# Optimization experiments

Measured on AMD Instinct MI355X. Metric: run time of the kernel, lower is better.

Reference implementation:

```python
import jax, jax.numpy as jnp
import numpy as np

D_MODEL = 256
NHEAD = 8
DHEAD = D_MODEL // NHEAD
LN_EPS = 1e-5
ATTN_EPS = 1e-6


def layer_norm(x, gamma, beta):
    mu = jnp.mean(x, axis=-1, keepdims=True)
    var = jnp.mean(jnp.square(x - mu), axis=-1, keepdims=True)
    return (x - mu) * jax.lax.rsqrt(var + LN_EPS) * gamma + beta


def setup_inputs() -> dict:
    key = jax.random.key(0)
    ks = jax.random.split(key, 12)
    B, L, S = 8, 4096, 4096
    s = 1.0 / np.sqrt(D_MODEL)
    return {
        "x": jax.random.normal(ks[0], (B, L, D_MODEL), jnp.float32),
        "source": jax.random.normal(ks[1], (B, S, D_MODEL), jnp.float32),
        "wq": jax.random.normal(ks[2], (D_MODEL, D_MODEL), jnp.float32) * s,
        "wk": jax.random.normal(ks[3], (D_MODEL, D_MODEL), jnp.float32) * s,
        "wv": jax.random.normal(ks[4], (D_MODEL, D_MODEL), jnp.float32) * s,
        "wmerge": jax.random.normal(ks[5], (D_MODEL, D_MODEL), jnp.float32) * s,
        "w1": jax.random.normal(ks[6], (2 * D_MODEL, D_MODEL), jnp.float32) * s,
        "w2": jax.random.normal(ks[7], (D_MODEL, 2 * D_MODEL), jnp.float32) * (1.0 / np.sqrt(2 * D_MODEL)),
        "g1": jnp.ones((D_MODEL,), jnp.float32),
        "b1": jnp.zeros((D_MODEL,), jnp.float32),
        "g2": jnp.ones((D_MODEL,), jnp.float32),
        "b2": jnp.zeros((D_MODEL,), jnp.float32),
    }


def reference(x, source, wq, wk, wv, wmerge, w1, w2, g1, b1, g2, b2):
    B, L, _ = x.shape
    S = source.shape[1]
    # QKV projections (bias-free Linear: y = x @ W^T), split into heads
    q = (x @ wq.T).reshape(B, L, NHEAD, DHEAD)
    k = (source @ wk.T).reshape(B, S, NHEAD, DHEAD)
    v = (source @ wv.T).reshape(B, S, NHEAD, DHEAD)
    # LinearAttention (LoFTR): feature map elu(.)+1, kernelized attention
    Q = jax.nn.elu(q) + 1.0
    K = jax.nn.elu(k) + 1.0
    v_len = jnp.asarray(S, v.dtype)
    values = v / v_len
    KV = jnp.einsum('bshd,bshv->bhdv', K, values)        # [B,H,D,D]
    Z = 1.0 / (jnp.einsum('blhd,bhd->blh', Q, K.sum(axis=1)) + ATTN_EPS)
    attended = jnp.einsum('blhd,bhdv,blh->blhv', Q, KV, Z) * v_len
    # merge + residual LN
    message = attended.reshape(B, L, D_MODEL) @ wmerge.T
    x = x + layer_norm(message, g1, b1)
    # MLP (d -> 2d -> d, ReLU) + residual LN
    h = jax.nn.relu(x @ w1.T) @ w2.T
    x = x + layer_norm(h, g2, b2)
    return x
```

## Files before the change

### kernel.cpp

```cpp
#include <hip/hip_runtime.h>
#include <hip/hip_bf16.h>

#define DM 256
#define SEQ 4096
#define XSTR 528
#define KSTR 144

typedef __attribute__((ext_vector_type(8))) short bf16x8;
typedef __attribute__((ext_vector_type(4))) float f32x4;

#define MFMA16(a, b, c) __builtin_amdgcn_mfma_f32_16x16x32_bf16(a, b, c, 0, 0, 0)

__device__ __forceinline__ short f2bf(float f) {
    union { __hip_bfloat16 h; short s; } u;
    u.h = __float2bfloat16(f);
    return u.s;
}
__device__ __forceinline__ float bf2f(short s) {
    union { unsigned u; float f; } c; c.u = ((unsigned)(unsigned short)s) << 16; return c.f;
}
__device__ __forceinline__ bf16x8 pack8(float4 a, float4 b) {
    bf16x8 r;
    r[0] = f2bf(a.x); r[1] = f2bf(a.y); r[2] = f2bf(a.z); r[3] = f2bf(a.w);
    r[4] = f2bf(b.x); r[5] = f2bf(b.y); r[6] = f2bf(b.z); r[7] = f2bf(b.w);
    return r;
}

__global__ __launch_bounds__(256) void kWconv(const float* __restrict__ wq, const float* __restrict__ wk,
                                              const float* __restrict__ wv, const float* __restrict__ wm,
                                              const float* __restrict__ w1, const float* __restrict__ w2,
                                              short* __restrict__ dstws, float* __restrict__ kva,
                                              float* __restrict__ ksum) {
    int blk = blockIdx.x;
    int gid = blk * 256 + threadIdx.x;
    kva[gid] = 0.f;
    if (gid < 2048) ksum[gid] = 0.f;
    const float* src; short* dst;
    if (blk < 32)       { src = wq; dst = dstws;          }
    else if (blk < 64)  { src = wk; dst = dstws + 65536;  blk -= 32; }
    else if (blk < 96)  { src = wv; dst = dstws + 131072; blk -= 64; }
    else if (blk < 128) { src = wm; dst = dstws + 196608; blk -= 96; }
    else if (blk < 192) { src = w1; dst = dstws + 262144; blk -= 128; }
    else                { src = w2; dst = dstws + 393216; blk -= 192; }
    int idx = (blk * 256 + threadIdx.x) * 8;
    float4 f0 = *(const float4*)(src + idx), f1 = *(const float4*)(src + idx + 4);
    *(bf16x8*)(dst + idx) = pack8(f0, f1);
}

__global__ __launch_bounds__(512, 4) void kA(const float* __restrict__ src,
                                             const short* __restrict__ wk, const short* __restrict__ wv,
                                             float* __restrict__ kva, float* __restrict__ ksum) {
    __shared__ char lds[73728];
    int t = threadIdx.x, lane = t & 63, w = t >> 6, r16 = lane & 15, g = lane >> 4;
    int b = blockIdx.x >> 6, blk = blockIdx.x & 63;
    const float* S = src + ((size_t)b * SEQ + blk * 64) * DM;
#pragma unroll
    for (int i = 0; i < 4; i++) {
        int chunk = t + i * 512, row = chunk >> 5, c8 = chunk & 31;
        const float* p = S + row * DM + c8 * 8;
        float4 f0 = *(const float4*)p, f1 = *(const float4*)(p + 4);
        *(bf16x8*)(lds + row * XSTR + c8 * 16) = pack8(f0, f1);
    }
    __syncthreads();
    f32x4 zz = {0.f, 0.f, 0.f, 0.f};
    f32x4 ak[4][2], av[4][2];
#pragma unroll
    for (int mi = 0; mi < 4; mi++)
#pragma unroll
        for (int ni = 0; ni < 2; ni++) { ak[mi][ni] = zz; av[mi][ni] = zz; }
    const char* aB0 = lds + r16 * XSTR + g * 16;
    const short* wkB0 = wk + (w * 32 + r16) * DM + g * 8;
    const short* wvB0 = wv + (w * 32 + r16) * DM + g * 8;
#pragma unroll
    for (int kt = 0; kt < 8; kt++) {
        bf16x8 A[4];
#pragma unroll
        for (int mi = 0; mi < 4; mi++)
            A[mi] = *(const bf16x8*)(aB0 + mi * (16 * XSTR) + kt * 64);
#pragma unroll
        for (int ni = 0; ni < 2; ni++) {
            bf16x8 Bk = *(const bf16x8*)(wkB0 + ni * (16 * DM) + kt * 32);
            bf16x8 Bv = *(const bf16x8*)(wvB0 + ni * (16 * DM) + kt * 32);
#pragma unroll
            for (int mi = 0; mi < 4; mi++) {
                ak[mi][ni] = MFMA16(A[mi], Bk, ak[mi][ni]);
                av[mi][ni] = MFMA16(A[mi], Bv, av[mi][ni]);
            }
        }
    }
    __syncthreads();
    char* kT = lds + w * 9216;
    char* vT = kT + 4608;
    float ksp[2] = {0.f, 0.f};
#pragma unroll
    for (int mi = 0; mi < 4; mi++)
#pragma unroll
        for (int ni = 0; ni < 2; ni++)
#pragma unroll
            for (int j = 0; j < 4; j++) {
                float q = ak[mi][ni][j];
                float e = q > 0.f ? q + 1.f : __expf(q);
                ksp[ni] += e;
                int srow = mi * 16 + g * 4 + j, feat = ni * 16 + r16;
                int by = feat * KSTR + srow * 2;
                *(short*)(kT + by) = f2bf(e);
                *(short*)(vT + by) = f2bf(av[mi][ni][j]);
            }
    __syncthreads();
    f32x4 kv[2][2];
#pragma unroll
    for (int vi = 0; vi < 2; vi++)
#pragma unroll
        for (int di = 0; di < 2; di++) kv[vi][di] = zz;
    {
        const char* vB = vT + r16 * KSTR + g * 16;
        const char* kB = kT + r16 * KSTR + g * 16;
#pragma unroll
        for (int st = 0; st < 2; st++) {
            bf16x8 Af[2], Bf[2];
#pragma unroll
            for (int vi = 0; vi < 2; vi++) {
                Af[vi] = *(const bf16x8*)(vB + vi * (16 * KSTR) + st * 64);
                Bf[vi] = *(const bf16x8*)(kB + vi * (16 * KSTR) + st * 64);
            }
#pragma unroll
            for (int vi = 0; vi < 2; vi++)
#pragma unroll
                for (int di = 0; di < 2; di++) kv[vi][di] = MFMA16(Af[vi], Bf[di], kv[vi][di]);
        }
    }
    float* kvp = kva + (size_t)(b * 8 + w) * 1024;
#pragma unroll
    for (int vi = 0; vi < 2; vi++)
#pragma unroll
        for (int di = 0; di < 2; di++)
#pragma unroll
            for (int j = 0; j < 4; j++) {
                int v = vi * 16 + g * 4 + j, d = di * 16 + r16;
                atomicAdd(&kvp[v * 32 + d], kv[vi][di][j]);
            }
#pragma unroll
    for (int ni = 0; ni < 2; ni++) {
        ksp[ni] += __shfl_xor(ksp[ni], 16);
        ksp[ni] += __shfl_xor(ksp[ni], 32);
    }
    if (lane < 16) {
#pragma unroll
        for (int ni = 0; ni < 2; ni++)
            atomicAdd(&ksum[(b * 8 + w) * 32 + ni * 16 + lane], ksp[ni]);
    }
}

__global__ __launch_bounds__(512, 4) void kBC(const float* __restrict__ x,
                                              const short* __restrict__ wq_bf, const short* __restrict__ wm_bf,
                                              const short* __restrict__ w1_bf, const short* __restrict__ w2_bf,
                                              const float* __restrict__ kva, const float* __restrict__ ksum,
                                              const float* __restrict__ g1, const float* __restrict__ b1,
                                              const float* __restrict__ g2, const float* __restrict__ b2,
                                              float* __restrict__ out) {
    __shared__ char lds[72704];
    char* xt = lds;
    char* qa = lds + 33792;
    float* red = (float*)(lds + 67584);
    float* ksl = (float*)(lds + 71680);
    int t = threadIdx.x, lane = t & 63, w = t >> 6, r16 = lane & 15, g = lane >> 4;
    int b = blockIdx.x >> 6, lb = blockIdx.x & 63, l0 = lb * 64;
    const float* xb = x + ((size_t)b * SEQ + l0) * DM;
#pragma unroll
    for (int i = 0; i < 4; i++) {
        int chunk = t + i * 512, row = chunk >> 5, c8 = chunk & 31;
        const float* p = xb + row * DM + c8 * 8;
        float4 f0 = *(const float4*)p, f1 = *(const float4*)(p + 4);
        *(bf16x8*)(xt + row * XSTR + c8 * 16) = pack8(f0, f1);
    }
    if (t < 256) ksl[t] = ksum[b * 256 + t];
    __syncthreads();
    f32x4 zz = {0.f, 0.f, 0.f, 0.f};
    const char* aXB = xt + r16 * XSTR + g * 16;
    const char* aQB = qa + r16 * XSTR + g * 16;
    f32x4 acc[4][2];
#pragma unroll
    for (int mi = 0; mi < 4; mi++)
#pragma unroll
        for (int ni = 0; ni < 2; ni++) acc[mi][ni] = zz;
    {
        const short* wqB = wq_bf + (w * 32 + r16) * DM + g * 8;
#pragma unroll
        for (int kt = 0; kt < 8; kt++) {
            bf16x8 A[4], Bf[2];
#pragma unroll
            for (int mi = 0; mi < 4; mi++)
                A[mi] = *(const bf16x8*)(aXB + mi * (16 * XSTR) + kt * 64);
#pragma unroll
            for (int ni = 0; ni < 2; ni++)
                Bf[ni] = *(const bf16x8*)(wqB + ni * (16 * DM) + kt * 32);
#pragma unroll
            for (int mi = 0; mi < 4; mi++)
#pragma unroll
                for (int ni = 0; ni < 2; ni++) acc[mi][ni] = MFMA16(A[mi], Bf[ni], acc[mi][ni]);
        }
    }
    float ks0 = ksl[w * 32 + r16], ks1 = ksl[w * 32 + 16 + r16];
    float Zr[4][4];
#pragma unroll
    for (int mi = 0; mi < 4; mi++)
#pragma unroll
        for (int j = 0; j < 4; j++) {
#pragma unroll
            for (int ni = 0; ni < 2; ni++) {
                float q = acc[mi][ni][j];
                acc[mi][ni][j] = q > 0.f ? q + 1.f : __expf(q);
            }
            float d0 = acc[mi][0][j] * ks0 + acc[mi][1][j] * ks1;
#pragma unroll
            for (int m = 1; m < 16; m <<= 1) d0 += __shfl_xor(d0, m);
            Zr[mi][j] = 1.f / (d0 + 1e-6f);
        }
#pragma unroll
    for (int mi = 0; mi < 4; mi++)
#pragma unroll
        for (int ni = 0; ni < 2; ni++)
#pragma unroll
            for (int j = 0; j < 4; j++) {
                int row = mi * 16 + g * 4 + j, col = w * 32 + ni * 16 + r16;
                *(short*)(qa + row * XSTR + col * 2) = f2bf(acc[mi][ni][j]);
            }
    f32x4 at[4][2];
#pragma unroll
    for (int mi = 0; mi < 4; mi++)
#pragma unroll
        for (int vi = 0; vi < 2; vi++) at[mi][vi] = zz;
    {
        bf16x8 A2[4], B2[2];
#pragma unroll
        for (int mi = 0; mi < 4; mi++)
            A2[mi] = *(const bf16x8*)(qa + (mi * 16 + r16) * XSTR + (w * 32 + g * 8) * 2);
        const float* kvb = kva + (size_t)(b * 8 + w) * 1024;
#pragma unroll
        for (int vi = 0; vi < 2; vi++) {
            const float* p = kvb + (vi * 16 + r16) * 32 + g * 8;
            float4 f0 = *(const float4*)p, f1 = *(const float4*)(p + 4);
            B2[vi] = pack8(f0, f1);
        }
#pragma unroll
        for (int mi = 0; mi < 4; mi++)
#pragma unroll
            for (int vi = 0; vi < 2; vi++) at[mi][vi] = MFMA16(A2[mi], B2[vi], at[mi][vi]);
    }
#pragma unroll
    for (int mi = 0; mi < 4; mi++)
#pragma unroll
        for (int vi = 0; vi < 2; vi++)
#pragma unroll
            for (int j = 0; j < 4; j++) {
                int row = mi * 16 + g * 4 + j, col = w * 32 + vi * 16 + r16;
                *(short*)(qa + row * XSTR + col * 2) = f2bf(at[mi][vi][j] * Zr[mi][j]);
            }
    __syncthreads();
    f32x4 am[4][2];
#pragma unroll
    for (int mi = 0; mi < 4; mi++)
#pragma unroll
        for (int ni = 0; ni < 2; ni++) am[mi][ni] = zz;
    {
        const short* wmB = wm_bf + (w * 32 + r16) * DM + g * 8;
#pragma unroll
        for (int kt = 0; kt < 8; kt++) {
            bf16x8 A[4], Bf[2];
#pragma unroll
            for (int mi = 0; mi < 4; mi++)
                A[mi] = *(const bf16x8*)(aQB + mi * (16 * XSTR) + kt * 64);
#pragma unroll
            for (int ni = 0; ni < 2; ni++)
                Bf[ni] = *(const bf16x8*)(wmB + ni * (16 * DM) + kt * 32);
#pragma unroll
            for (int mi = 0; mi < 4; mi++)
#pragma unroll
                for (int ni = 0; ni < 2; ni++) am[mi][ni] = MFMA16(A[mi], Bf[ni], am[mi][ni]);
        }
    }
#pragma unroll
    for (int mi = 0; mi < 4; mi++)
#pragma unroll
        for (int j = 0; j < 4; j++) {
            float s = am[mi][0][j] + am[mi][1][j];
            float s2 = am[mi][0][j] * am[mi][0][j] + am[mi][1][j] * am[mi][1][j];
#pragma unroll
            for (int m = 1; m < 16; m <<= 1) { s += __shfl_xor(s, m); s2 += __shfl_xor(s2, m); }
            if (r16 == 0) { int row = mi * 16 + g * 4 + j; red[(row * 8 + w) * 2] = s; red[(row * 8 + w) * 2 + 1] = s2; }
        }
    __syncthreads();
    {
        float g1v[2], b1v[2];
#pragma unroll
        for (int ni = 0; ni < 2; ni++) { int col = w * 32 + ni * 16 + r16; g1v[ni] = g1[col]; b1v[ni] = b1[col]; }
#pragma unroll
        for (int mi = 0; mi < 4; mi++)
#pragma unroll
            for (int j = 0; j < 4; j++) {
                int row = mi * 16 + g * 4 + j;
                float mu = 0.f, ex2 = 0.f;
#pragma unroll
                for (int ww = 0; ww < 8; ww++) { mu += red[(row * 8 + ww) * 2]; ex2 += red[(row * 8 + ww) * 2 + 1]; }
                mu *= (1.f / DM); ex2 *= (1.f / DM);
                float rstd = rsqrtf(ex2 - mu * mu + 1e-5f);
#pragma unroll
                for (int ni = 0; ni < 2; ni++) {
                    int col = w * 32 + ni * 16 + r16;
                    char* bp = xt + row * XSTR + col * 2;
                    float xv = bf2f(*(const short*)bp);
                    *(short*)bp = f2bf(xv + (am[mi][ni][j] - mu) * rstd * g1v[ni] + b1v[ni]);
                }
            }
    }
    __syncthreads();
    f32x4 a2[4][2];
#pragma unroll
    for (int mi = 0; mi < 4; mi++)
#pragma unroll
        for (int ni = 0; ni < 2; ni++) a2[mi][ni] = zz;
#pragma unroll
    for (int hf = 0; hf < 2; hf++) {
        f32x4 a1[4][2];
#pragma unroll
        for (int mi = 0; mi < 4; mi++)
#pragma unroll
            for (int ni = 0; ni < 2; ni++) a1[mi][ni] = zz;
        {
            const short* w1B = w1_bf + (hf * 256 + w * 32 + r16) * DM + g * 8;
#pragma unroll
            for (int kt = 0; kt < 8; kt++) {
                bf16x8 A[4], Bf[2];
#pragma unroll
                for (int mi = 0; mi < 4; mi++)
                    A[mi] = *(const bf16x8*)(aXB + mi * (16 * XSTR) + kt * 64);
#pragma unroll
                for (int ni = 0; ni < 2; ni++)
                    Bf[ni] = *(const bf16x8*)(w1B + ni * (16 * DM) + kt * 32);
#pragma unroll
                for (int mi = 0; mi < 4; mi++)
#pragma unroll
                    for (int ni = 0; ni < 2; ni++) a1[mi][ni] = MFMA16(A[mi], Bf[ni], a1[mi][ni]);
            }
        }
#pragma unroll
        for (int mi = 0; mi < 4; mi++)
#pragma unroll
            for (int ni = 0; ni < 2; ni++)
#pragma unroll
                for (int j = 0; j < 4; j++) {
                    float hv = a1[mi][ni][j]; hv = hv > 0.f ? hv : 0.f;
                    int row = mi * 16 + g * 4 + j, col = w * 32 + ni * 16 + r16;
                    *(short*)(qa + row * XSTR + col * 2) = f2bf(hv);
                }
        __syncthreads();
        {
            const short* w2B = w2_bf + (w * 32 + r16) * 512 + hf * 256 + g * 8;
#pragma unroll
            for (int kt = 0; kt < 8; kt++) {
                bf16x8 A[4], Bf[2];
#pragma unroll
                for (int mi = 0; mi < 4; mi++)
                    A[mi] = *(const bf16x8*)(aQB + mi * (16 * XSTR) + kt * 64);
#pragma unroll
                for (int ni = 0; ni < 2; ni++)
                    Bf[ni] = *(const bf16x8*)(w2B + ni * (16 * 512) + kt * 32);
#pragma unroll
                for (int mi = 0; mi < 4; mi++)
#pragma unroll
                    for (int ni = 0; ni < 2; ni++) a2[mi][ni] = MFMA16(A[mi], Bf[ni], a2[mi][ni]);
            }
        }
        __syncthreads();
    }
#pragma unroll
    for (int mi = 0; mi < 4; mi++)
#pragma unroll
        for (int j = 0; j < 4; j++) {
            float s = a2[mi][0][j] + a2[mi][1][j];
            float s2 = a2[mi][0][j] * a2[mi][0][j] + a2[mi][1][j] * a2[mi][1][j];
#pragma unroll
            for (int m = 1; m < 16; m <<= 1) { s += __shfl_xor(s, m); s2 += __shfl_xor(s2, m); }
            if (r16 == 0) { int row = mi * 16 + g * 4 + j; red[(row * 8 + w) * 2] = s; red[(row * 8 + w) * 2 + 1] = s2; }
        }
    __syncthreads();
    {
        float g2v[2], b2v[2];
#pragma unroll
        for (int ni = 0; ni < 2; ni++) { int col = w * 32 + ni * 16 + r16; g2v[ni] = g2[col]; b2v[ni] = b2[col]; }
        float* op = out + ((size_t)b * SEQ + l0) * DM;
#pragma unroll
        for (int mi = 0; mi < 4; mi++)
#pragma unroll
            for (int j = 0; j < 4; j++) {
                int row = mi * 16 + g * 4 + j;
                float mu = 0.f, ex2 = 0.f;
#pragma unroll
                for (int ww = 0; ww < 8; ww++) { mu += red[(row * 8 + ww) * 2]; ex2 += red[(row * 8 + ww) * 2 + 1]; }
                mu *= (1.f / DM); ex2 *= (1.f / DM);
                float rstd = rsqrtf(ex2 - mu * mu + 1e-5f);
#pragma unroll
                for (int ni = 0; ni < 2; ni++) {
                    int col = w * 32 + ni * 16 + r16;
                    float xv = bf2f(*(const short*)(xt + row * XSTR + col * 2));
                    op[row * DM + col] = xv + (a2[mi][ni][j] - mu) * rstd * g2v[ni] + b2v[ni];
                }
            }
    }
}

extern "C" void kernel_launch(void* const* d_in, const int* in_sizes, int n_in,
                              void* d_out, int out_size, void* d_ws, size_t ws_size,
                              hipStream_t stream) {
    const float* x   = (const float*)d_in[0];
    const float* src = (const float*)d_in[1];
    const float* wq  = (const float*)d_in[2];
    const float* wk  = (const float*)d_in[3];
    const float* wv  = (const float*)d_in[4];
    const float* wm  = (const float*)d_in[5];
    const float* w1  = (const float*)d_in[6];
    const float* w2  = (const float*)d_in[7];
    const float* g1  = (const float*)d_in[8];
    const float* b1  = (const float*)d_in[9];
    const float* g2  = (const float*)d_in[10];
    const float* b2  = (const float*)d_in[11];
    float* out = (float*)d_out;

    char* ws = (char*)d_ws;
    short* w_bf = (short*)ws;
    float* kva  = (float*)(ws + 1048576);
    float* ksum = (float*)(ws + 1310720);

    kWconv<<<256, 256, 0, stream>>>(wq, wk, wv, wm, w1, w2, w_bf, kva, ksum);
    kA<<<512, 512, 0, stream>>>(src, w_bf + 65536, w_bf + 131072, kva, ksum);
    kBC<<<512, 512, 0, stream>>>(x, w_bf, w_bf + 196608, w_bf + 262144, w_bf + 393216,
                                 kva, ksum, g1, b1, g2, b2, out);
}
```

Measured before the change: 218.0 us.

## Halve kA row tile, prefetch weight fragments in kBC GEMMs, inline bf16 rounding

```diff
diff --git a/kernel.cpp b/kernel.cpp
--- a/kernel.cpp
+++ b/kernel.cpp
@@ -4,7 +4,7 @@
 #define DM 256
 #define SEQ 4096
 #define XSTR 528
-#define KSTR 144
+#define TSTR 72
 
 typedef __attribute__((ext_vector_type(8))) short bf16x8;
 typedef __attribute__((ext_vector_type(4))) float f32x4;
@@ -12,9 +12,9 @@
 #define MFMA16(a, b, c) __builtin_amdgcn_mfma_f32_16x16x32_bf16(a, b, c, 0, 0, 0)
 
 __device__ __forceinline__ short f2bf(float f) {
-    union { __hip_bfloat16 h; short s; } u;
-    u.h = __float2bfloat16(f);
-    return u.s;
+    union { float f; unsigned u; } c; c.f = f;
+    unsigned r = (c.u + 0x7FFFu + ((c.u >> 16) & 1u)) >> 16;
+    return (short)r;
 }
 __device__ __forceinline__ float bf2f(short s) {
     union { unsigned u; float f; } c; c.u = ((unsigned)(unsigned short)s) << 16; return c.f;
@@ -50,12 +50,12 @@
 __global__ __launch_bounds__(512, 4) void kA(const float* __restrict__ src,
                                              const short* __restrict__ wk, const short* __restrict__ wv,
                                              float* __restrict__ kva, float* __restrict__ ksum) {
-    __shared__ char lds[73728];
+    __shared__ char lds[36864];
     int t = threadIdx.x, lane = t & 63, w = t >> 6, r16 = lane & 15, g = lane >> 4;
-    int b = blockIdx.x >> 6, blk = blockIdx.x & 63;
-    const float* S = src + ((size_t)b * SEQ + blk * 64) * DM;
-#pragma unroll
-    for (int i = 0; i < 4; i++) {
+    int b = blockIdx.x >> 7, blk = blockIdx.x & 127;
+    const float* S = src + ((size_t)b * SEQ + blk * 32) * DM;
+#pragma unroll
+    for (int i = 0; i < 2; i++) {
         int chunk = t + i * 512, row = chunk >> 5, c8 = chunk & 31;
         const float* p = S + row * DM + c8 * 8;
         float4 f0 = *(const float4*)p, f1 = *(const float4*)(p + 4);
@@ -63,9 +63,9 @@
     }
     __syncthreads();
     f32x4 zz = {0.f, 0.f, 0.f, 0.f};
-    f32x4 ak[4][2], av[4][2];
-#pragma unroll
-    for (int mi = 0; mi < 4; mi++)
+    f32x4 ak[2][2], av[2][2];
+#pragma unroll
+    for (int mi = 0; mi < 2; mi++)
 #pragma unroll
         for (int ni = 0; ni < 2; ni++) { ak[mi][ni] = zz; av[mi][ni] = zz; }
     const char* aB0 = lds + r16 * XSTR + g * 16;
@@ -73,27 +73,27 @@
     const short* wvB0 = wv + (w * 32 + r16) * DM + g * 8;
 #pragma unroll
     for (int kt = 0; kt < 8; kt++) {
-        bf16x8 A[4];
-#pragma unroll
-        for (int mi = 0; mi < 4; mi++)
+        bf16x8 A[2];
+#pragma unroll
+        for (int mi = 0; mi < 2; mi++)
             A[mi] = *(const bf16x8*)(aB0 + mi * (16 * XSTR) + kt * 64);
 #pragma unroll
         for (int ni = 0; ni < 2; ni++) {
             bf16x8 Bk = *(const bf16x8*)(wkB0 + ni * (16 * DM) + kt * 32);
             bf16x8 Bv = *(const bf16x8*)(wvB0 + ni * (16 * DM) + kt * 32);
 #pragma unroll
-            for (int mi = 0; mi < 4; mi++) {
+            for (int mi = 0; mi < 2; mi++) {
                 ak[mi][ni] = MFMA16(A[mi], Bk, ak[mi][ni]);
                 av[mi][ni] = MFMA16(A[mi], Bv, av[mi][ni]);
             }
         }
     }
     __syncthreads();
-    char* kT = lds + w * 9216;
-    char* vT = kT + 4608;
+    char* kT = lds + w * 4608;
+    char* vT = kT + 2304;
     float ksp[2] = {0.f, 0.f};
 #pragma unroll
-    for (int mi = 0; mi < 4; mi++)
+    for (int mi = 0; mi < 2; mi++)
 #pragma unroll
         for (int ni = 0; ni < 2; ni++)
 #pragma unroll
@@ -102,7 +102,7 @@
                 float e = q > 0.f ? q + 1.f : __expf(q);
                 ksp[ni] += e;
                 int srow = mi * 16 + g * 4 + j, feat = ni * 16 + r16;
-                int by = feat * KSTR + srow * 2;
+                int by = feat * TSTR + srow * 2;
                 *(short*)(kT + by) = f2bf(e);
                 *(short*)(vT + by) = f2bf(av[mi][ni][j]);
             }
@@ -113,21 +113,16 @@
 #pragma unroll
         for (int di = 0; di < 2; di++) kv[vi][di] = zz;
     {
-        const char* vB = vT + r16 * KSTR + g * 16;
-        const char* kB = kT + r16 * KSTR + g * 16;
-#pragma unroll
-        for (int st = 0; st < 2; st++) {
-            bf16x8 Af[2], Bf[2];
-#pragma unroll
-            for (int vi = 0; vi < 2; vi++) {
-                Af[vi] = *(const bf16x8*)(vB + vi * (16 * KSTR) + st * 64);
-                Bf[vi] = *(const bf16x8*)(kB + vi * (16 * KSTR) + st * 64);
-            }
-#pragma unroll
-            for (int vi = 0; vi < 2; vi++)
-#pragma unroll
-                for (int di = 0; di < 2; di++) kv[vi][di] = MFMA16(Af[vi], Bf[di], kv[vi][di]);
-        }
+        bf16x8 Af[2], Bf[2];
+#pragma unroll
+        for (int vi = 0; vi < 2; vi++) {
+            Af[vi] = *(const bf16x8*)(vT + (vi * 16 + r16) * TSTR + g * 16);
+            Bf[vi] = *(const bf16x8*)(kT + (vi * 16 + r16) * TSTR + g * 16);
+        }
+#pragma unroll
+        for (int vi = 0; vi < 2; vi++)
+#pragma unroll
+            for (int di = 0; di < 2; di++) kv[vi][di] = MFMA16(Af[vi], Bf[di], kv[vi][di]);
     }
     float* kvp = kva + (size_t)(b * 8 + w) * 1024;
 #pragma unroll
@@ -185,19 +180,25 @@
         for (int ni = 0; ni < 2; ni++) acc[mi][ni] = zz;
     {
         const short* wqB = wq_bf + (w * 32 + r16) * DM + g * 8;
+        bf16x8 B0 = *(const bf16x8*)(wqB);
+        bf16x8 B1 = *(const bf16x8*)(wqB + 16 * DM);
 #pragma unroll
         for (int kt = 0; kt < 8; kt++) {
-            bf16x8 A[4], Bf[2];
+            bf16x8 Bn0 = B0, Bn1 = B1;
+            if (kt < 7) {
+                Bn0 = *(const bf16x8*)(wqB + (kt + 1) * 32);
+                Bn1 = *(const bf16x8*)(wqB + 16 * DM + (kt + 1) * 32);
+            }
+            bf16x8 A[4];
 #pragma unroll
             for (int mi = 0; mi < 4; mi++)
                 A[mi] = *(const bf16x8*)(aXB + mi * (16 * XSTR) + kt * 64);
 #pragma unroll
-            for (int ni = 0; ni < 2; ni++)
-                Bf[ni] = *(const bf16x8*)(wqB + ni * (16 * DM) + kt * 32);
-#pragma unroll
-            for (int mi = 0; mi < 4; mi++)
-#pragma unroll
-                for (int ni = 0; ni < 2; ni++) acc[mi][ni] = MFMA16(A[mi], Bf[ni], acc[mi][ni]);
+            for (int mi = 0; mi < 4; mi++) {
+                acc[mi][0] = MFMA16(A[mi], B0, acc[mi][0]);
+                acc[mi][1] = MFMA16(A[mi], B1, acc[mi][1]);
+            }
+            B0 = Bn0; B1 = Bn1;
         }
     }
     float ks0 = ksl[w * 32 + r16], ks1 = ksl[w * 32 + 16 + r16];
@@ -264,19 +265,25 @@
         for (int ni = 0; ni < 2; ni++) am[mi][ni] = zz;
     {
         const short* wmB = wm_bf + (w * 32 + r16) * DM + g * 8;
+        bf16x8 B0 = *(const bf16x8*)(wmB);
+        bf16x8 B1 = *(const bf16x8*)(wmB + 16 * DM);
 #pragma unroll
         for (int kt = 0; kt < 8; kt++) {
-            bf16x8 A[4], Bf[2];
+            bf16x8 Bn0 = B0, Bn1 = B1;
+            if (kt < 7) {
+                Bn0 = *(const bf16x8*)(wmB + (kt + 1) * 32);
+                Bn1 = *(const bf16x8*)(wmB + 16 * DM + (kt + 1) * 32);
+            }
+            bf16x8 A[4];
 #pragma unroll
             for (int mi = 0; mi < 4; mi++)
                 A[mi] = *(const bf16x8*)(aQB + mi * (16 * XSTR) + kt * 64);
 #pragma unroll
-            for (int ni = 0; ni < 2; ni++)
-                Bf[ni] = *(const bf16x8*)(wmB + ni * (16 * DM) + kt * 32);
-#pragma unroll
-            for (int mi = 0; mi < 4; mi++)
-#pragma unroll
-                for (int ni = 0; ni < 2; ni++) am[mi][ni] = MFMA16(A[mi], Bf[ni], am[mi][ni]);
+            for (int mi = 0; mi < 4; mi++) {
+                am[mi][0] = MFMA16(A[mi], B0, am[mi][0]);
+                am[mi][1] = MFMA16(A[mi], B1, am[mi][1]);
+            }
+            B0 = Bn0; B1 = Bn1;
         }
     }
 #pragma unroll
@@ -328,19 +335,25 @@
             for (int ni = 0; ni < 2; ni++) a1[mi][ni] = zz;
         {
             const short* w1B = w1_bf + (hf * 256 + w * 32 + r16) * DM + g * 8;
+            bf16x8 B0 = *(const bf16x8*)(w1B);
+            bf16x8 B1 = *(const bf16x8*)(w1B + 16 * DM);
 #pragma unroll
             for (int kt = 0; kt < 8; kt++) {
-                bf16x8 A[4], Bf[2];
+                bf16x8 Bn0 = B0, Bn1 = B1;
+                if (kt < 7) {
+                    Bn0 = *(const bf16x8*)(w1B + (kt + 1) * 32);
+                    Bn1 = *(const bf16x8*)(w1B + 16 * DM + (kt + 1) * 32);
+                }
+                bf16x8 A[4];
 #pragma unroll
                 for (int mi = 0; mi < 4; mi++)
                     A[mi] = *(const bf16x8*)(aXB + mi * (16 * XSTR) + kt * 64);
 #pragma unroll
-                for (int ni = 0; ni < 2; ni++)
-                    Bf[ni] = *(const bf16x8*)(w1B + ni * (16 * DM) + kt * 32);
-#pragma unroll
-                for (int mi = 0; mi < 4; mi++)
-#pragma unroll
-                    for (int ni = 0; ni < 2; ni++) a1[mi][ni] = MFMA16(A[mi], Bf[ni], a1[mi][ni]);
+                for (int mi = 0; mi < 4; mi++) {
+                    a1[mi][0] = MFMA16(A[mi], B0, a1[mi][0]);
+                    a1[mi][1] = MFMA16(A[mi], B1, a1[mi][1]);
+                }
+                B0 = Bn0; B1 = Bn1;
             }
         }
 #pragma unroll
@@ -356,19 +369,25 @@
         __syncthreads();
         {
             const short* w2B = w2_bf + (w * 32 + r16) * 512 + hf * 256 + g * 8;
+            bf16x8 B0 = *(const bf16x8*)(w2B);
+            bf16x8 B1 = *(const bf16x8*)(w2B + 16 * 512);
 #pragma unroll
             for (int kt = 0; kt < 8; kt++) {
-                bf16x8 A[4], Bf[2];
+                bf16x8 Bn0 = B0, Bn1 = B1;
+                if (kt < 7) {
+                    Bn0 = *(const bf16x8*)(w2B + (kt + 1) * 32);
+                    Bn1 = *(const bf16x8*)(w2B + 16 * 512 + (kt + 1) * 32);
+                }
+                bf16x8 A[4];
 #pragma unroll
                 for (int mi = 0; mi < 4; mi++)
                     A[mi] = *(const bf16x8*)(aQB + mi * (16 * XSTR) + kt * 64);
 #pragma unroll
-                for (int ni = 0; ni < 2; ni++)
-                    Bf[ni] = *(const bf16x8*)(w2B + ni * (16 * 512) + kt * 32);
-#pragma unroll
-                for (int mi = 0; mi < 4; mi++)
-#pragma unroll
-                    for (int ni = 0; ni < 2; ni++) a2[mi][ni] = MFMA16(A[mi], Bf[ni], a2[mi][ni]);
+                for (int mi = 0; mi < 4; mi++) {
+                    a2[mi][0] = MFMA16(A[mi], B0, a2[mi][0]);
+                    a2[mi][1] = MFMA16(A[mi], B1, a2[mi][1]);
+                }
+                B0 = Bn0; B1 = Bn1;
             }
         }
         __syncthreads();
@@ -432,7 +451,7 @@
     float* ksum = (float*)(ws + 1310720);
 
     kWconv<<<256, 256, 0, stream>>>(wq, wk, wv, wm, w1, w2, w_bf, kva, ksum);
-    kA<<<512, 512, 0, stream>>>(src, w_bf + 65536, w_bf + 131072, kva, ksum);
+    kA<<<1024, 512, 0, stream>>>(src, w_bf + 65536, w_bf + 131072, kva, ksum);
     kBC<<<512, 512, 0, stream>>>(x, w_bf, w_bf + 196608, w_bf + 262144, w_bf + 393216,
                                  kva, ksum, g1, b1, g2, b2, out);
 }
```

Measured after the change: 242.9 us. +11.4%, slower.
